# Performance work log

Measured on AMD Instinct MI355X. Metric: run time of the kernel, lower is better.

## Reference

```python
import jax, jax.numpy as jnp
import numpy as np

INPUT_DIM = 8
TIMESTEPS = 4096
BATCH = 1024


def setup_inputs() -> dict:
    key = jax.random.key(0)
    k1, k2, k3 = jax.random.split(key, 3)
    x = jax.random.normal(k1, (BATCH, TIMESTEPS, INPUT_DIM), dtype=jnp.float32)
    # sklearn MinMaxScaler attributes; keep scale_ bounded away from zero
    min_ = jax.random.uniform(k2, (INPUT_DIM,), dtype=jnp.float32)
    scale_ = jax.random.uniform(k3, (INPUT_DIM,), dtype=jnp.float32) * 0.9 + 0.1
    return {"x": x, "min_": min_, "scale_": scale_}


def reference(x, min_, scale_):
    D = x.shape[-1]
    # inverse MinMax transform: (x - min_) / scale_ per feature column
    x_inv = (x.reshape(-1, D) - min_) / scale_  # (N, D), N = B*T

    device_and_status = x_inv[:, 2]    # (N,)
    activity_and_status = x_inv[:, 3]  # (N,)

    in_range = (device_and_status >= 0.0) & (device_and_status <= 252.0)
    device_and_status_penalty = jnp.sum(jnp.where(in_range, 0.0, 1.0))

    is_out_of_range = (activity_and_status < 0.0) | (activity_and_status > 22.0)
    activity_and_status_penalty = jnp.sum(is_out_of_range.astype(jnp.float32))

    # sequential transition scan, vectorized: the while_loop body is a pure
    # function of (a[i-1], a[i]) with a scalar branch -> shifted compare.
    prev = activity_and_status[:-1]
    cur = activity_and_status[1:]
    cond = (jnp.mod(prev, 2.0) == 0.0) & (prev < 20.0)
    invalid = (cur != prev + 1.0) & (cur != 22.0)
    invalid_transition_penalty = jnp.sum(
        jnp.where(cond, invalid.astype(jnp.float32), 0.0)
    )

    num_activities = jnp.sum((activity_and_status != 22.0).astype(jnp.float32))
    activity_count_penalty = jnp.abs(num_activities - 58.0)

    return (device_and_status_penalty + activity_and_status_penalty
            + invalid_transition_penalty + activity_count_penalty)
```

## Files before the change

### kernel.cpp

```cpp
#include <hip/hip_runtime.h>
#include <math.h>

#define NROWS (1024 * 4096)
#define BLOCKS 2048
#define TPB 256
#define R 8
#define NW (TPB / 64)

__global__ __launch_bounds__(TPB) void penalty_main(
        const float* __restrict__ x,
        const float* __restrict__ min_,
        const float* __restrict__ scale_,
        unsigned int* __restrict__ part) {
    const float min2 = min_[2], min3 = min_[3];
    const float sc2  = scale_[2], sc3 = scale_[3];

    const int tid  = threadIdx.x;
    const int lane = tid & 63;
    const int wave = tid >> 6;
    const unsigned T = BLOCKS * TPB;
    const unsigned t = blockIdx.x * TPB + tid;

    float2 v[R];
    #pragma unroll
    for (int r = 0; r < R; ++r) {
        v[r] = *(const float2*)(x + 8u * (t + (unsigned)r * T) + 2u);
    }

    float a[R];
    unsigned c1 = 0, c2 = 0, c4 = 0;
    #pragma unroll
    for (int r = 0; r < R; ++r) {
        const float d = (v[r].x - min2) / sc2;
        a[r] = (v[r].y - min3) / sc3;
        c1 += !(d >= 0.0f && d <= 252.0f);
        c2 += (a[r] < 0.0f) || (a[r] > 22.0f);
        c4 += (a[r] != 22.0f);
    }

    __shared__ float sA[NW][R];
    if (lane == 0) {
        #pragma unroll
        for (int r = 0; r < R; ++r) sA[wave][r] = a[r];
    }
    __syncthreads();

    float abound[R];
    if (tid == TPB - 1) {
        #pragma unroll
        for (int r = 0; r < R; ++r) {
            const unsigned j = t + (unsigned)r * T + 1u;
            abound[r] = (j < NROWS) ? (x[8u * j + 3u] - min3) / sc3 : 0.0f;
        }
    }

    unsigned c3 = 0;
    #pragma unroll
    for (int r = 0; r < R; ++r) {
        float an = __shfl_down(a[r], 1);
        if (lane == 63) an = (wave < NW - 1) ? sA[wave + 1][r] : abound[r];
        const unsigned i = t + (unsigned)r * T;
        const bool cond = (fmodf(a[r], 2.0f) == 0.0f) && (a[r] < 20.0f)
                          && (i + 1u < NROWS);
        const bool invalid = (an != a[r] + 1.0f) && (an != 22.0f);
        c3 += (cond && invalid);
    }

    for (int off = 32; off > 0; off >>= 1) {
        c1 += __shfl_down(c1, off);
        c2 += __shfl_down(c2, off);
        c3 += __shfl_down(c3, off);
        c4 += __shfl_down(c4, off);
    }
    __shared__ unsigned int s[NW][4];
    if (lane == 0) { s[wave][0] = c1; s[wave][1] = c2; s[wave][2] = c3; s[wave][3] = c4; }
    __syncthreads();
    if (tid == 0) {
        unsigned t1 = 0, t2 = 0, t3 = 0, t4 = 0;
        #pragma unroll
        for (int w = 0; w < NW; ++w) {
            t1 += s[w][0]; t2 += s[w][1]; t3 += s[w][2]; t4 += s[w][3];
        }
        unsigned int* p = part + 4u * blockIdx.x;
        p[0] = t1; p[1] = t2; p[2] = t3; p[3] = t4;
    }
}

__global__ __launch_bounds__(TPB) void finalize(
        const unsigned int* __restrict__ part, float* __restrict__ out) {
    const int tid = threadIdx.x;
    unsigned c1 = 0, c2 = 0, c3 = 0, c4 = 0;
    for (int b = tid; b < BLOCKS; b += TPB) {
        const unsigned int* p = part + 4 * b;
        c1 += p[0]; c2 += p[1]; c3 += p[2]; c4 += p[3];
    }
    for (int off = 32; off > 0; off >>= 1) {
        c1 += __shfl_down(c1, off);
        c2 += __shfl_down(c2, off);
        c3 += __shfl_down(c3, off);
        c4 += __shfl_down(c4, off);
    }
    __shared__ unsigned int s[NW][4];
    const int lane = tid & 63, wave = tid >> 6;
    if (lane == 0) { s[wave][0] = c1; s[wave][1] = c2; s[wave][2] = c3; s[wave][3] = c4; }
    __syncthreads();
    if (tid == 0) {
        unsigned t1 = 0, t2 = 0, t3 = 0, t4 = 0;
        #pragma unroll
        for (int w = 0; w < NW; ++w) {
            t1 += s[w][0]; t2 += s[w][1]; t3 += s[w][2]; t4 += s[w][3];
        }
        out[0] = (float)t1 + (float)t2 + (float)t3
               + fabsf((float)t4 - 58.0f);
    }
}

extern "C" void kernel_launch(void* const* d_in, const int* in_sizes, int n_in,
                              void* d_out, int out_size, void* d_ws, size_t ws_size,
                              hipStream_t stream) {
    const float* x  = (const float*)d_in[0];
    const float* mn = (const float*)d_in[1];
    const float* sc = (const float*)d_in[2];
    unsigned int* part = (unsigned int*)d_ws;
    float* out = (float*)d_out;

    penalty_main<<<BLOCKS, TPB, 0, stream>>>(x, mn, sc, part);
    finalize<<<1, TPB, 0, stream>>>(part, out);
}
```

Measured before the change: 202.5 us.

## Load full rows as float4 pairs and fuse finalize via last-block atomics

Each thread now loads both 16-byte halves of every 32-byte row as two float4 loads instead of an 8-byte float2 slice, keeping the unused half alive with a dummy sum so the loads are not removed. The aim is full-line coalesced access. The grid doubles while rows per thread halve, and the fmodf test is replaced by a floor-based parity check. The separate finalize kernel is replaced by per-block atomics plus a last-block-done counter, with a memset of the workspace before launch, which adds a memset and atomic contention.

```diff
diff --git a/kernel.cpp b/kernel.cpp
--- a/kernel.cpp
+++ b/kernel.cpp
@@ -1,17 +1,19 @@
 #include <hip/hip_runtime.h>
 #include <math.h>
 
-#define NROWS (1024 * 4096)
-#define BLOCKS 2048
-#define TPB 256
-#define R 8
-#define NW (TPB / 64)
+#define NROWS  (1024 * 4096)
+#define BLOCKS 4096
+#define TPB    256
+#define R      4
+#define NW     (TPB / 64)
+
 
 __global__ __launch_bounds__(TPB) void penalty_main(
         const float* __restrict__ x,
         const float* __restrict__ min_,
         const float* __restrict__ scale_,
-        unsigned int* __restrict__ part) {
+        unsigned int* __restrict__ ws,
+        float* __restrict__ out) {
     const float min2 = min_[2], min3 = min_[3];
     const float sc2  = scale_[2], sc3 = scale_[3];
 
@@ -21,22 +23,28 @@
     const unsigned T = BLOCKS * TPB;
     const unsigned t = blockIdx.x * TPB + tid;
 
-    float2 v[R];
+    const float4* __restrict__ x4 = (const float4*)x;
+    float4 lo[R], hi[R];
     #pragma unroll
-    for (int r = 0; r < R; ++r) {
-        v[r] = *(const float2*)(x + 8u * (t + (unsigned)r * T) + 2u);
-    }
+    for (int r = 0; r < R; ++r) lo[r] = x4[2u * (t + (unsigned)r * T)];
+    #pragma unroll
+    for (int r = 0; r < R; ++r) hi[r] = x4[2u * (t + (unsigned)r * T) + 1u];
 
     float a[R];
     unsigned c1 = 0, c2 = 0, c4 = 0;
     #pragma unroll
     for (int r = 0; r < R; ++r) {
-        const float d = (v[r].x - min2) / sc2;
-        a[r] = (v[r].y - min3) / sc3;
+        const float d = (lo[r].z - min2) / sc2;
+        a[r] = (lo[r].w - min3) / sc3;
         c1 += !(d >= 0.0f && d <= 252.0f);
         c2 += (a[r] < 0.0f) || (a[r] > 22.0f);
         c4 += (a[r] != 22.0f);
     }
+
+    float dummy = 0.0f;
+    #pragma unroll
+    for (int r = 0; r < R; ++r) dummy += hi[r].x + hi[r].y + hi[r].z + hi[r].w;
+    c1 += (dummy * 0.0f != 0.0f);
 
     __shared__ float sA[NW][R];
     if (lane == 0) {
@@ -60,8 +68,8 @@
         float an = __shfl_down(a[r], 1);
         if (lane == 63) an = (wave < NW - 1) ? sA[wave + 1][r] : abound[r];
         const unsigned i = t + (unsigned)r * T;
-        const bool cond = (fmodf(a[r], 2.0f) == 0.0f) && (a[r] < 20.0f)
-                          && (i + 1u < NROWS);
+        const float h = 0.5f * a[r];
+        const bool cond = (h == floorf(h)) && (a[r] < 20.0f) && (i + 1u < NROWS);
         const bool invalid = (an != a[r] + 1.0f) && (an != 22.0f);
         c3 += (cond && invalid);
     }
@@ -75,43 +83,28 @@
     __shared__ unsigned int s[NW][4];
     if (lane == 0) { s[wave][0] = c1; s[wave][1] = c2; s[wave][2] = c3; s[wave][3] = c4; }
     __syncthreads();
+
     if (tid == 0) {
         unsigned t1 = 0, t2 = 0, t3 = 0, t4 = 0;
         #pragma unroll
         for (int w = 0; w < NW; ++w) {
             t1 += s[w][0]; t2 += s[w][1]; t3 += s[w][2]; t4 += s[w][3];
         }
-        unsigned int* p = part + 4u * blockIdx.x;
-        p[0] = t1; p[1] = t2; p[2] = t3; p[3] = t4;
-    }
-}
-
-__global__ __launch_bounds__(TPB) void finalize(
-        const unsigned int* __restrict__ part, float* __restrict__ out) {
-    const int tid = threadIdx.x;
-    unsigned c1 = 0, c2 = 0, c3 = 0, c4 = 0;
-    for (int b = tid; b < BLOCKS; b += TPB) {
-        const unsigned int* p = part + 4 * b;
-        c1 += p[0]; c2 += p[1]; c3 += p[2]; c4 += p[3];
-    }
-    for (int off = 32; off > 0; off >>= 1) {
-        c1 += __shfl_down(c1, off);
-        c2 += __shfl_down(c2, off);
-        c3 += __shfl_down(c3, off);
-        c4 += __shfl_down(c4, off);
-    }
-    __shared__ unsigned int s[NW][4];
-    const int lane = tid & 63, wave = tid >> 6;
-    if (lane == 0) { s[wave][0] = c1; s[wave][1] = c2; s[wave][2] = c3; s[wave][3] = c4; }
-    __syncthreads();
-    if (tid == 0) {
-        unsigned t1 = 0, t2 = 0, t3 = 0, t4 = 0;
-        #pragma unroll
-        for (int w = 0; w < NW; ++w) {
-            t1 += s[w][0]; t2 += s[w][1]; t3 += s[w][2]; t4 += s[w][3];
+        atomicAdd(&ws[0],  t1);
+        atomicAdd(&ws[32], t2);
+        atomicAdd(&ws[64], t3);
+        atomicAdd(&ws[96], t4);
+        __threadfence();
+        const unsigned old = atomicAdd(&ws[128], 1u);
+        if (old == BLOCKS - 1) {
+            __threadfence();
+            const unsigned f1 = atomicAdd(&ws[0],  0u);
+            const unsigned f2 = atomicAdd(&ws[32], 0u);
+            const unsigned f3 = atomicAdd(&ws[64], 0u);
+            const unsigned f4 = atomicAdd(&ws[96], 0u);
+            out[0] = (float)f1 + (float)f2 + (float)f3
+                   + fabsf((float)f4 - 58.0f);
         }
-        out[0] = (float)t1 + (float)t2 + (float)t3
-               + fabsf((float)t4 - 58.0f);
     }
 }
 
@@ -121,9 +114,9 @@
     const float* x  = (const float*)d_in[0];
     const float* mn = (const float*)d_in[1];
     const float* sc = (const float*)d_in[2];
-    unsigned int* part = (unsigned int*)d_ws;
+    unsigned int* ws = (unsigned int*)d_ws;
     float* out = (float*)d_out;
 
-    penalty_main<<<BLOCKS, TPB, 0, stream>>>(x, mn, sc, part);
-    finalize<<<1, TPB, 0, stream>>>(part, out);
+    hipMemsetAsync(ws, 0, 129 * sizeof(unsigned int), stream);
+    penalty_main<<<BLOCKS, TPB, 0, stream>>>(x, mn, sc, ws, out);
 }
```

Result: slower. 355.1 us (+75.4%).
